# Performance work log

Measured on AMD Instinct MI355X. Metric: run time of the kernel, lower is better.

## Reference

```python
import jax, jax.numpy as jnp
import numpy as np

N, H, W = 64, 384, 384
ITERATIONS = 5

_PLUS = jnp.array([[0., 1., 0.], [1., 1., 1.], [0., 1., 0.]], dtype=jnp.float32)


def _dilate(x, kernel):
    # morphological dilation: conv2d with plus kernel, padding=1, clamp to [0,1]
    out = jax.lax.conv_general_dilated(
        x, kernel,
        window_strides=(1, 1), padding='SAME',
        dimension_numbers=('NCHW', 'OIHW', 'NCHW'))
    return jnp.clip(out, 0.0, 1.0)


def setup_inputs() -> dict:
    key = jax.random.key(0)
    k1, k2, k3 = jax.random.split(key, 3)
    hand_mask = jax.random.uniform(k1, (N, 1, H, W), dtype=jnp.float32)
    object_mask = jax.random.uniform(k2, (N, 1, H, W), dtype=jnp.float32)
    target = jax.random.uniform(k3, (N, 1, H, W), dtype=jnp.float32)
    return {"hand_mask": hand_mask, "object_mask": object_mask, "target": target}


def reference(hand_mask, object_mask, target):
    kernel = _PLUS[None, None]  # (1,1,3,3) OIHW
    h, o = hand_mask, object_mask
    for _ in range(ITERATIONS):
        h = _dilate(h, kernel)
        o = _dilate(o, kernel)
    p = h * o  # contact boundary probability, in [0,1]
    # F.binary_cross_entropy clamps log terms at -100
    log_p = jnp.maximum(jnp.log(p), -100.0)
    log_1mp = jnp.maximum(jnp.log(1.0 - p), -100.0)
    loss = -jnp.mean(target * log_p + (1.0 - target) * log_1mp)
    return loss
```

## Files before the change

### kernel.cpp

```cpp
#include <hip/hip_runtime.h>

#define IMG   384
#define NIMG  64
#define HALO  5
#define NW    4
#define RW    10
#define TH    (NW*RW)
#define VY    (TH - 2*HALO)
#define VX    116
#define GRIDX 4
#define GRIDY 13
#define NPART (GRIDX*GRIDY*NIMG)

typedef float f32x2 __attribute__((ext_vector_type(2)));

static __device__ __forceinline__ f32x2 pk_add(f32x2 a, f32x2 b) {
    f32x2 d; asm("v_pk_add_f32 %0, %1, %2" : "=v"(d) : "v"(a), "v"(b)); return d;
}
static __device__ __forceinline__ f32x2 pk_add_swap(f32x2 a, f32x2 b) {
    f32x2 d; asm("v_pk_add_f32 %0, %1, %2 op_sel:[0,1] op_sel_hi:[1,0]"
                 : "=v"(d) : "v"(a), "v"(b)); return d;
}
static __device__ __forceinline__ f32x2 pk_mul(f32x2 a, f32x2 b) {
    f32x2 d; asm("v_pk_mul_f32 %0, %1, %2" : "=v"(d) : "v"(a), "v"(b)); return d;
}
static __device__ __forceinline__ float dpp_sr1(float x) {
    return __int_as_float(
        __builtin_amdgcn_update_dpp(0, __float_as_int(x), 0x138, 0xF, 0xF, true));
}
static __device__ __forceinline__ float dpp_sl1(float x) {
    return __int_as_float(
        __builtin_amdgcn_update_dpp(0, __float_as_int(x), 0x130, 0xF, 0xF, true));
}

__global__ __launch_bounds__(256, 4) void boundary_bce_fused(
    const float* __restrict__ hand,
    const float* __restrict__ obj,
    const float* __restrict__ target,
    float* __restrict__ partial)
{
    const int tid  = threadIdx.x;
    const int lane = tid & 63;
    const int w    = tid >> 6;
    const int tx = blockIdx.x, ty = blockIdx.y, n = blockIdx.z;

    const int x0    = tx * VX - 6;
    const int y0    = ty * VY - HALO;
    const int gx0   = x0 + 2 * lane;
    const int ybase = y0 + w * RW;

    const size_t ioff = (size_t)n * IMG * IMG;
    const float* __restrict__ hp = hand   + ioff;
    const float* __restrict__ op = obj    + ioff;
    const float* __restrict__ tp = target + ioff;

    const bool colok = (gx0 >= 0) & (gx0 < IMG);
    const float mc   = colok ? 1.f : 0.f;
    const f32x2 mcol = {mc, mc};
    const f32x2 zero = {0.f, 0.f};

    f32x2 h[RW], o[RW];
    #pragma unroll
    for (int r = 0; r < RW; ++r) {
        int gy = ybase + r;
        bool ok = colok & (gy >= 0) & (gy < IMG);
        size_t idx = (size_t)gy * IMG + gx0;
        h[r] = ok ? *(const f32x2*)(hp + idx) : zero;
        o[r] = ok ? *(const f32x2*)(op + idx) : zero;
    }

    const bool ztop = (ty == 0)         && (w == 0);
    const bool zbot = (ty == GRIDY - 1) && (w == 2);

    __shared__ f32x2 sTopH[2][NW][64], sBotH[2][NW][64];
    __shared__ f32x2 sTopO[2][NW][64], sBotO[2][NW][64];

    #pragma unroll 1
    for (int it = 0; it < 5; ++it) {
        const int b = it & 1;
        sTopH[b][w][lane] = h[0];  sBotH[b][w][lane] = h[RW-1];
        sTopO[b][w][lane] = o[0];  sBotO[b][w][lane] = o[RW-1];
        __syncthreads();

        f32x2 upH = (w > 0)      ? sBotH[b][w-1][lane] : zero;
        f32x2 upO = (w > 0)      ? sBotO[b][w-1][lane] : zero;
        f32x2 dnH = (w < NW - 1) ? sTopH[b][w+1][lane] : zero;
        f32x2 dnO = (w < NW - 1) ? sTopO[b][w+1][lane] : zero;

        f32x2 prevH = upH, prevO = upO;
        #pragma unroll
        for (int r = 0; r < RW; ++r) {
            f32x2 belowH = (r == RW - 1) ? dnH : h[r+1];
            f32x2 belowO = (r == RW - 1) ? dnO : o[r+1];
            f32x2 cH = h[r], cO = o[r];
            f32x2 vH = pk_add(pk_add(cH, prevH), belowH);
            f32x2 vO = pk_add(pk_add(cO, prevO), belowO);
            f32x2 sH = pk_add_swap(vH, cH);
            f32x2 sO = pk_add_swap(vO, cO);
            sH.x += dpp_sr1(cH.y); sH.y += dpp_sl1(cH.x);
            sO.x += dpp_sr1(cO.y); sO.y += dpp_sl1(cO.x);
            sH.x = fminf(sH.x, 1.f); sH.y = fminf(sH.y, 1.f);
            sO.x = fminf(sO.x, 1.f); sO.y = fminf(sO.y, 1.f);
            h[r] = pk_mul(sH, mcol);
            o[r] = pk_mul(sO, mcol);
            prevH = cH; prevO = cO;
        }
        if (ztop) { h[4] = zero; o[4] = zero; }
        if (zbot) { h[9] = zero; o[9] = zero; }
    }

    const float C = -144.26950408889634f;
    float psum = 0.f;
    const bool lane_ok = colok & (lane >= 3) & (lane <= 60);
    #pragma unroll
    for (int r = 0; r < RW; ++r) {
        int ly = w * RW + r;
        int gy = ybase + r;
        bool v = lane_ok & (ly >= HALO) & (ly <= TH - 1 - HALO) & (gy < IMG);
        if (v) {
            f32x2 p = pk_mul(h[r], o[r]);
            f32x2 t = *(const f32x2*)(tp + (size_t)gy * IMG + gx0);
            float lp0  = fmaxf(__log2f(p.x),       C);
            float l1p0 = fmaxf(__log2f(1.f - p.x), C);
            float lp1  = fmaxf(__log2f(p.y),       C);
            float l1p1 = fmaxf(__log2f(1.f - p.y), C);
            psum += t.x * lp0 + (1.f - t.x) * l1p0;
            psum += t.y * lp1 + (1.f - t.y) * l1p1;
        }
    }

    #pragma unroll
    for (int off = 32; off > 0; off >>= 1)
        psum += __shfl_down(psum, off, 64);
    __shared__ float wsum[NW];
    if (lane == 0) wsum[w] = psum;
    __syncthreads();
    if (tid == 0) {
        partial[blockIdx.x + GRIDX * (blockIdx.y + GRIDY * blockIdx.z)] =
            wsum[0] + wsum[1] + wsum[2] + wsum[3];
    }
}

__global__ __launch_bounds__(256) void boundary_bce_finalize(
    const float* __restrict__ partial, float* __restrict__ out)
{
    float s = 0.f;
    for (int i = threadIdx.x; i < NPART; i += 256) s += partial[i];
    #pragma unroll
    for (int off = 32; off > 0; off >>= 1)
        s += __shfl_down(s, off, 64);
    __shared__ float ws[4];
    if ((threadIdx.x & 63) == 0) ws[threadIdx.x >> 6] = s;
    __syncthreads();
    if (threadIdx.x == 0) {
        const float LN2 = 0.69314718055994531f;
        float tot = ws[0] + ws[1] + ws[2] + ws[3];
        out[0] = -(tot * LN2) / (float)((size_t)NIMG * IMG * IMG);
    }
}

extern "C" void kernel_launch(void* const* d_in, const int* in_sizes, int n_in,
                              void* d_out, int out_size, void* d_ws, size_t ws_size,
                              hipStream_t stream)
{
    const float* hand   = (const float*)d_in[0];
    const float* obj    = (const float*)d_in[1];
    const float* target = (const float*)d_in[2];
    float* partial = (float*)d_ws;

    dim3 grid(GRIDX, GRIDY, NIMG);
    boundary_bce_fused<<<grid, 256, 0, stream>>>(hand, obj, target, partial);
    boundary_bce_finalize<<<1, 256, 0, stream>>>(partial, (float*)d_out);
}
```

Baseline: 146.5 us.

## Give each wave independent haloed row strip, drop LDS halo exchange and barriers

Each wavefront now loads its own 12 output rows plus a 5-row halo on each side into registers and runs the five dilation steps on a shrinking window. This removes the per-iteration shared-memory halo exchange and the __syncthreads barriers. Partial sums are written per wave, so the block-level reduction goes away. Interior column tiles use a template specialization that skips column masking. In exchange the kernel does redundant halo loads and compute, and the 22-row register arrays raise register pressure, which may lower occupancy.

```diff
diff --git a/kernel.cpp b/kernel.cpp
--- a/kernel.cpp
+++ b/kernel.cpp
@@ -2,15 +2,13 @@
 
 #define IMG   384
 #define NIMG  64
-#define HALO  5
+#define RWV   12
+#define RL    (RWV + 10)
 #define NW    4
-#define RW    10
-#define TH    (NW*RW)
-#define VY    (TH - 2*HALO)
 #define VX    116
 #define GRIDX 4
-#define GRIDY 13
-#define NPART (GRIDX*GRIDY*NIMG)
+#define GRIDY 8
+#define NPART (GRIDX*GRIDY*NIMG*NW)
 
 typedef float f32x2 __attribute__((ext_vector_type(2)));
 
@@ -33,91 +31,73 @@
         __builtin_amdgcn_update_dpp(0, __float_as_int(x), 0x130, 0xF, 0xF, true));
 }
 
-__global__ __launch_bounds__(256, 4) void boundary_bce_fused(
-    const float* __restrict__ hand,
-    const float* __restrict__ obj,
-    const float* __restrict__ target,
-    float* __restrict__ partial)
+template<bool EDGE>
+static __device__ __forceinline__ void dilate_bce(
+    const float* __restrict__ hp, const float* __restrict__ op,
+    const float* __restrict__ tp, float* __restrict__ partial,
+    int tx, int ty, int n, int lane, int wu)
 {
-    const int tid  = threadIdx.x;
-    const int lane = tid & 63;
-    const int w    = tid >> 6;
-    const int tx = blockIdx.x, ty = blockIdx.y, n = blockIdx.z;
+    const int x0    = tx * VX - 6;
+    const int gx0   = x0 + 2 * lane;
+    const int vy0   = ty * (NW * RWV) + wu * RWV;
+    const int ybase = vy0 - 5;
 
-    const int x0    = tx * VX - 6;
-    const int y0    = ty * VY - HALO;
-    const int gx0   = x0 + 2 * lane;
-    const int ybase = y0 + w * RW;
-
-    const size_t ioff = (size_t)n * IMG * IMG;
-    const float* __restrict__ hp = hand   + ioff;
-    const float* __restrict__ op = obj    + ioff;
-    const float* __restrict__ tp = target + ioff;
-
-    const bool colok = (gx0 >= 0) & (gx0 < IMG);
-    const float mc   = colok ? 1.f : 0.f;
-    const f32x2 mcol = {mc, mc};
-    const f32x2 zero = {0.f, 0.f};
-
-    f32x2 h[RW], o[RW];
-    #pragma unroll
-    for (int r = 0; r < RW; ++r) {
-        int gy = ybase + r;
-        bool ok = colok & (gy >= 0) & (gy < IMG);
-        size_t idx = (size_t)gy * IMG + gx0;
-        h[r] = ok ? *(const f32x2*)(hp + idx) : zero;
-        o[r] = ok ? *(const f32x2*)(op + idx) : zero;
+    bool colok = true;
+    f32x2 mcol = {1.f, 1.f};
+    int gxs = gx0;
+    if (EDGE) {
+        colok = (gx0 >= 0) & (gx0 < IMG);
+        mcol.x = mcol.y = colok ? 1.f : 0.f;
+        gxs = colok ? gx0 : 0;
     }
 
-    const bool ztop = (ty == 0)         && (w == 0);
-    const bool zbot = (ty == GRIDY - 1) && (w == 2);
+    const f32x2 zero = {0.f, 0.f};
+    f32x2 h[RL], o[RL];
+    #pragma unroll
+    for (int r = 0; r < RL; ++r) {
+        const int gy = ybase + r;
+        if (gy >= 0 && gy < IMG) {
+            const size_t idx = (size_t)gy * IMG + gxs;
+            f32x2 hv = *(const f32x2*)(hp + idx);
+            f32x2 ov = *(const f32x2*)(op + idx);
+            h[r] = EDGE ? pk_mul(hv, mcol) : hv;
+            o[r] = EDGE ? pk_mul(ov, mcol) : ov;
+        } else { h[r] = zero; o[r] = zero; }
+    }
 
-    __shared__ f32x2 sTopH[2][NW][64], sBotH[2][NW][64];
-    __shared__ f32x2 sTopO[2][NW][64], sBotO[2][NW][64];
+    const bool ztop = (ty == 0)         && (wu == 0);
+    const bool zbot = (ty == GRIDY - 1) && (wu == NW - 1);
 
-    #pragma unroll 1
-    for (int it = 0; it < 5; ++it) {
-        const int b = it & 1;
-        sTopH[b][w][lane] = h[0];  sBotH[b][w][lane] = h[RW-1];
-        sTopO[b][w][lane] = o[0];  sBotO[b][w][lane] = o[RW-1];
-        __syncthreads();
-
-        f32x2 upH = (w > 0)      ? sBotH[b][w-1][lane] : zero;
-        f32x2 upO = (w > 0)      ? sBotO[b][w-1][lane] : zero;
-        f32x2 dnH = (w < NW - 1) ? sTopH[b][w+1][lane] : zero;
-        f32x2 dnO = (w < NW - 1) ? sTopO[b][w+1][lane] : zero;
-
-        f32x2 prevH = upH, prevO = upO;
+    #pragma unroll
+    for (int it = 1; it <= 5; ++it) {
+        f32x2 prevH = h[it-1], prevO = o[it-1];
         #pragma unroll
-        for (int r = 0; r < RW; ++r) {
-            f32x2 belowH = (r == RW - 1) ? dnH : h[r+1];
-            f32x2 belowO = (r == RW - 1) ? dnO : o[r+1];
+        for (int r = it; r <= RL - 1 - it; ++r) {
             f32x2 cH = h[r], cO = o[r];
-            f32x2 vH = pk_add(pk_add(cH, prevH), belowH);
-            f32x2 vO = pk_add(pk_add(cO, prevO), belowO);
+            f32x2 vH = pk_add(pk_add(cH, prevH), h[r+1]);
+            f32x2 vO = pk_add(pk_add(cO, prevO), o[r+1]);
             f32x2 sH = pk_add_swap(vH, cH);
             f32x2 sO = pk_add_swap(vO, cO);
             sH.x += dpp_sr1(cH.y); sH.y += dpp_sl1(cH.x);
             sO.x += dpp_sr1(cO.y); sO.y += dpp_sl1(cO.x);
             sH.x = fminf(sH.x, 1.f); sH.y = fminf(sH.y, 1.f);
             sO.x = fminf(sO.x, 1.f); sO.y = fminf(sO.y, 1.f);
-            h[r] = pk_mul(sH, mcol);
-            o[r] = pk_mul(sO, mcol);
+            if (EDGE) { sH = pk_mul(sH, mcol); sO = pk_mul(sO, mcol); }
+            h[r] = sH; o[r] = sO;
             prevH = cH; prevO = cO;
         }
-        if (ztop) { h[4] = zero; o[4] = zero; }
-        if (zbot) { h[9] = zero; o[9] = zero; }
+        if (ztop) { h[4]    = zero; o[4]    = zero; }
+        if (zbot) { h[RL-5] = zero; o[RL-5] = zero; }
     }
 
     const float C = -144.26950408889634f;
     float psum = 0.f;
-    const bool lane_ok = colok & (lane >= 3) & (lane <= 60);
-    #pragma unroll
-    for (int r = 0; r < RW; ++r) {
-        int ly = w * RW + r;
-        int gy = ybase + r;
-        bool v = lane_ok & (ly >= HALO) & (ly <= TH - 1 - HALO) & (gy < IMG);
-        if (v) {
+    bool lane_ok = (lane >= 3) & (lane <= 60);
+    if (EDGE) lane_ok = lane_ok & colok;
+    if (lane_ok) {
+        #pragma unroll
+        for (int r = 5; r <= RL - 6; ++r) {
+            const int gy = ybase + r;
             f32x2 p = pk_mul(h[r], o[r]);
             f32x2 t = *(const f32x2*)(tp + (size_t)gy * IMG + gx0);
             float lp0  = fmaxf(__log2f(p.x),       C);
@@ -132,13 +112,30 @@
     #pragma unroll
     for (int off = 32; off > 0; off >>= 1)
         psum += __shfl_down(psum, off, 64);
-    __shared__ float wsum[NW];
-    if (lane == 0) wsum[w] = psum;
-    __syncthreads();
-    if (tid == 0) {
-        partial[blockIdx.x + GRIDX * (blockIdx.y + GRIDY * blockIdx.z)] =
-            wsum[0] + wsum[1] + wsum[2] + wsum[3];
-    }
+    if (lane == 0)
+        partial[(((size_t)n * GRIDY + ty) * GRIDX + tx) * NW + wu] = psum;
+}
+
+__global__ __launch_bounds__(256, 4) void boundary_bce_fused(
+    const float* __restrict__ hand,
+    const float* __restrict__ obj,
+    const float* __restrict__ target,
+    float* __restrict__ partial)
+{
+    const int tid  = threadIdx.x;
+    const int lane = tid & 63;
+    const int wu   = __builtin_amdgcn_readfirstlane(tid >> 6);
+    const int tx = blockIdx.x, ty = blockIdx.y, n = blockIdx.z;
+
+    const size_t ioff = (size_t)n * IMG * IMG;
+    const float* hp = hand   + ioff;
+    const float* op = obj    + ioff;
+    const float* tp = target + ioff;
+
+    if (tx == 0 || tx == GRIDX - 1)
+        dilate_bce<true >(hp, op, tp, partial, tx, ty, n, lane, wu);
+    else
+        dilate_bce<false>(hp, op, tp, partial, tx, ty, n, lane, wu);
 }
 
 __global__ __launch_bounds__(256) void boundary_bce_finalize(
```

New measurement: 159.9 us. 1.09x slower.
